# Performance work log

Hardware: AMD Instinct MI355X
Metric: run time of the kernel (lower is better)

Reference implementation:

```python
import jax, jax.numpy as jnp
import numpy as np

POS_MARGIN = 0.01
NEG_MARGIN = 0.2
REG_WEIGHT = 0.1
N, D = 8192, 256
NUM_CLASSES = 512


def setup_inputs() -> dict:
    key = jax.random.key(0)
    k1, k2 = jax.random.split(key)
    embeds = jax.random.normal(k1, (N, D), dtype=jnp.float32)
    labels = jax.random.randint(k2, (N,), 0, NUM_CLASSES, dtype=jnp.int64)
    return {"embeds": embeds, "labels": labels}


def reference(embeds, labels):
    n, d = embeds.shape
    # L2-normalize embeddings (normalize_embeds=True)
    e = embeds / jnp.linalg.norm(embeds, axis=1, keepdims=True)

    # var(e_i - e_j, ddof=1) over feature dim, computed without the [N,N,D] tensor:
    # var = (D/(D-1)) * ( mean(e_i^2) + mean(e_j^2) - 2*mean(e_i*e_j) - (m_i - m_j)^2 )
    m = e.mean(axis=1)                      # [N]
    s = (e * e).mean(axis=1)                # [N]
    g = (e @ e.T) / d                       # [N,N] = mean(e_i * e_j) over D
    corr = d / (d - 1.0)
    var_diff = corr * (s[:, None] + s[None, :] - 2.0 * g - (m[:, None] - m[None, :]) ** 2)
    row_var = corr * (s - m * m)            # torch.var(e, dim=1), unbiased
    distmat = var_diff / row_var[:, None]

    same = labels[:, None] == labels[None, :]
    eye = jnp.eye(n, dtype=bool)
    pos_mask = same & (~eye)                # all same-label pairs (anchor != positive)
    neg_mask = ~same                        # all diff-label pairs

    pos_l = jax.nn.relu(distmat - POS_MARGIN) * pos_mask
    neg_l = jax.nn.relu(NEG_MARGIN - distmat) * neg_mask

    # avg_nonzero_only=True: sum / (# strictly-positive entries + 1e-12)
    pos_loss = pos_l.sum() / ((pos_l > 0).sum().astype(jnp.float32) + 1e-12)
    neg_loss = neg_l.sum() / ((neg_l > 0).sum().astype(jnp.float32) + 1e-12)

    loss = pos_loss + neg_loss
    loss = loss + jnp.abs(e.sum(axis=1)).mean() * REG_WEIGHT
    return loss
```

## Files before the change

kernel.cpp:

```cpp
#include <hip/hip_runtime.h>

#define NROWS 8192
#define DDIM 256
#define BT 128
#define BK 32
#define GT (NROWS / BT)
#define NBT (GT * (GT + 1) / 2)

using bf16x8 = __attribute__((ext_vector_type(8))) __bf16;
using f32x4  = __attribute__((ext_vector_type(4))) float;

__device__ __forceinline__ void glds16(const unsigned short* g, unsigned short* l) {
    __builtin_amdgcn_global_load_lds(
        (const __attribute__((address_space(1))) unsigned int*)g,
        (__attribute__((address_space(3))) unsigned int*)l,
        16, 0, 0);
}

__device__ __forceinline__ unsigned short f2bf(float f) {
    unsigned int b = __float_as_uint(f);
    unsigned int r = b + 0x7fffu + ((b >> 16) & 1u);
    return (unsigned short)(r >> 16);
}

__global__ __launch_bounds__(256) void rowstats_kernel(
    const float* __restrict__ x, unsigned short* __restrict__ ebf,
    float* __restrict__ aP, float* __restrict__ bs,
    float* __restrict__ rabs)
{
    int wave = threadIdx.x >> 6;
    int lane = threadIdx.x & 63;
    int row  = blockIdx.x * 4 + wave;

    const float4 v = reinterpret_cast<const float4*>(x + (size_t)row * DDIM)[lane];
    float ss = v.x * v.x + v.y * v.y + v.z * v.z + v.w * v.w;
    float sm = v.x + v.y + v.z + v.w;
    #pragma unroll
    for (int off = 32; off >= 1; off >>= 1) {
        ss += __shfl_xor(ss, off);
        sm += __shfl_xor(sm, off);
    }
    float invn = 1.0f / sqrtf(ss);
    float m = sm * invn * (1.0f / DDIM);

    ushort4 o;
    o.x = f2bf(v.x * invn - m);
    o.y = f2bf(v.y * invn - m);
    o.z = f2bf(v.z * invn - m);
    o.w = f2bf(v.w * invn - m);
    reinterpret_cast<ushort4*>(ebf + (size_t)row * DDIM)[lane] = o;

    if (lane == 0) {
        float s  = ss * invn * invn * (1.0f / DDIM);
        float b  = s - m * m;
        float a  = 1.0f / b;
        aP[row]   = a * (1.0f / 128.0f);
        bs[row]   = -128.0f * b;
        rabs[row] = fabsf(sm * invn);
    }
}

__global__ __launch_bounds__(256) void snr_gemm_kernel(
    const unsigned short* __restrict__ ebf,
    const float* __restrict__ aP, const float* __restrict__ bs,
    const int* __restrict__ labels,
    float* __restrict__ partials)
{
    __shared__ __align__(16) unsigned short As[BT * BK];
    __shared__ __align__(16) unsigned short Bs[BT * BK];
    __shared__ float sAPi[BT], sBsi[BT];
    __shared__ float sAPj[BT], sBsj[BT];
    __shared__ int   sLi[BT], sLj[BT];
    __shared__ float redbuf[4][4];

    int tid  = threadIdx.x;
    int lane = tid & 63;
    int wave = tid >> 6;
    int wr = (wave >> 1) * 64;
    int wc = (wave & 1) * 64;

    int t = blockIdx.x;
    int bi = (int)((2.0f * GT + 1.0f
                    - sqrtf((2.0f * GT + 1.0f) * (2.0f * GT + 1.0f) - 8.0f * (float)t)) * 0.5f);
    while ((bi + 1) * GT - ((bi + 1) * bi) / 2 <= t) ++bi;
    while (bi * GT - (bi * (bi - 1)) / 2 > t) --bi;
    int bj = bi + (t - (bi * GT - (bi * (bi - 1)) / 2));
    int rowBase = bi * BT, colBase = bj * BT;
    bool diag = (bi == bj);

    if (tid < BT) {
        int gi = rowBase + tid;
        sAPi[tid] = aP[gi]; sBsi[tid] = bs[gi];
        sLi[tid] = labels[gi];
    } else {
        int tt = tid - BT;
        int gj = colBase + tt;
        sAPj[tt] = aP[gj]; sBsj[tt] = bs[gj];
        sLj[tt] = labels[gj];
    }

    const unsigned short* gA[2];
    const unsigned short* gB[2];
    unsigned short* lpA[2];
    unsigned short* lpB[2];
    #pragma unroll
    for (int p = 0; p < 2; ++p) {
        int q   = p * 256 + tid;
        int row = q >> 2;
        int kc  = (q & 3) ^ (row & 3) ^ ((row >> 2) & 3);
        gA[p] = ebf + (size_t)(rowBase + row) * DDIM + kc * 8;
        gB[p] = ebf + (size_t)(colBase + row) * DDIM + kc * 8;
        lpA[p] = As + q * 8;
        lpB[p] = Bs + q * 8;
    }

    int mrow = lane & 15;
    int kch  = lane >> 4;
    int offA[4], offB[4];
    #pragma unroll
    for (int t4 = 0; t4 < 4; ++t4) {
        int rA = wr + t4 * 16 + mrow;
        int rB = wc + t4 * 16 + mrow;
        offA[t4] = (rA * 4 + (kch ^ (rA & 3) ^ ((rA >> 2) & 3))) * 8;
        offB[t4] = (rB * 4 + (kch ^ (rB & 3) ^ ((rB >> 2) & 3))) * 8;
    }

    f32x4 acc[4][4];
    #pragma unroll
    for (int a = 0; a < 4; ++a)
        #pragma unroll
        for (int b = 0; b < 4; ++b)
            acc[a][b] = (f32x4){0.f, 0.f, 0.f, 0.f};

    for (int it = 0; it < 8; ++it) {
        #pragma unroll
        for (int p = 0; p < 2; ++p) {
            glds16(gA[p], lpA[p]);
            glds16(gB[p], lpB[p]);
            gA[p] += BK;
            gB[p] += BK;
        }
        asm volatile("s_waitcnt vmcnt(0)" ::: "memory");
        __syncthreads();

        bf16x8 aF[4], bF[4];
        #pragma unroll
        for (int t4 = 0; t4 < 4; ++t4) {
            aF[t4] = *reinterpret_cast<const bf16x8*>(As + offA[t4]);
            bF[t4] = *reinterpret_cast<const bf16x8*>(Bs + offB[t4]);
        }
        #pragma unroll
        for (int ti = 0; ti < 4; ++ti)
            #pragma unroll
            for (int tj = 0; tj < 4; ++tj)
                acc[ti][tj] = __builtin_amdgcn_mfma_f32_16x16x32_bf16(aF[ti], bF[tj], acc[ti][tj], 0, 0, 0);
        __syncthreads();
    }

    int subr = (lane >> 4) * 4;
    int cj   = lane & 15;

    float aPC[4], bsC[4];
    int LCj[4];
    #pragma unroll
    for (int tj = 0; tj < 4; ++tj) {
        int lj = wc + tj * 16 + cj;
        aPC[tj] = sAPj[lj]; bsC[tj] = sBsj[lj];
        LCj[tj] = sLj[lj];
    }

    float Sn = 0.f, Sp = 0.f;
    unsigned Cn = 0u, Cp = 0u;

    if (!diag) {
        #pragma unroll
        for (int ti = 0; ti < 4; ++ti) {
            #pragma unroll
            for (int r = 0; r < 4; ++r) {
                int li = wr + ti * 16 + subr + r;
                float aR = sAPi[li], bR = sBsi[li];
                int LR = sLi[li];
                #pragma unroll
                for (int tj = 0; tj < 4; ++tj) {
                    float raw = acc[ti][tj][r];
                    float v1 = fmaf(aR, raw + bsC[tj], -0.8f);
                    float v2 = fmaf(aPC[tj], raw + bR, -0.8f);
                    bool same = (LR == LCj[tj]);
                    unsigned long long ms = __ballot(same);
                    float nz = fmaxf(v1, 0.f) + fmaxf(v2, 0.f);
                    Sn += same ? 0.f : nz;
                    float pz = fmaxf(0.19f - v1, 0.f) + fmaxf(0.19f - v2, 0.f);
                    Sp += same ? pz : 0.f;
                    Cn += (unsigned)__popcll(__ballot(v1 > 0.f) & ~ms)
                        + (unsigned)__popcll(__ballot(v2 > 0.f) & ~ms);
                    Cp += (unsigned)__popcll(__ballot(v1 < 0.19f) & ms)
                        + (unsigned)__popcll(__ballot(v2 < 0.19f) & ms);
                }
            }
        }
    } else {
        #pragma unroll
        for (int ti = 0; ti < 4; ++ti) {
            #pragma unroll
            for (int r = 0; r < 4; ++r) {
                int li = wr + ti * 16 + subr + r;
                float aR = sAPi[li];
                int LR = sLi[li];
                #pragma unroll
                for (int tj = 0; tj < 4; ++tj) {
                    int lj = wc + tj * 16 + cj;
                    float raw = acc[ti][tj][r];
                    float v1 = fmaf(aR, raw + bsC[tj], -0.8f);
                    bool same = (LR == LCj[tj]);
                    bool pok  = same && (li != lj);
                    unsigned long long ms = __ballot(same);
                    unsigned long long mp = __ballot(pok);
                    Sn += same ? 0.f : fmaxf(v1, 0.f);
                    float pz = fmaxf(0.19f - v1, 0.f);
                    Sp += pok ? pz : 0.f;
                    Cn += (unsigned)__popcll(__ballot(v1 > 0.f) & ~ms);
                    Cp += (unsigned)__popcll(__ballot(v1 < 0.19f) & mp);
                }
            }
        }
    }

    #pragma unroll
    for (int off = 32; off >= 1; off >>= 1) {
        Sn += __shfl_down(Sn, off);
        Sp += __shfl_down(Sp, off);
    }
    if (lane == 0) {
        redbuf[wave][0] = Sn; redbuf[wave][1] = (float)Cn;
        redbuf[wave][2] = Sp; redbuf[wave][3] = (float)Cp;
    }
    __syncthreads();
    if (tid < 4) {
        partials[blockIdx.x * 4 + tid] =
            redbuf[0][tid] + redbuf[1][tid] + redbuf[2][tid] + redbuf[3][tid];
    }
}

__global__ __launch_bounds__(256) void finalize_kernel(
    const float* __restrict__ partials, const float* __restrict__ rabs,
    float* __restrict__ out)
{
    int tid = threadIdx.x;
    float s0 = 0, s1 = 0, s2 = 0, s3 = 0, rr = 0;
    for (int i = tid; i < NBT; i += 256) {
        float4 p = reinterpret_cast<const float4*>(partials)[i];
        s0 += p.x; s1 += p.y; s2 += p.z; s3 += p.w;
    }
    for (int i = tid; i < NROWS; i += 256) rr += rabs[i];

    #pragma unroll
    for (int off = 32; off >= 1; off >>= 1) {
        s0 += __shfl_down(s0, off);
        s1 += __shfl_down(s1, off);
        s2 += __shfl_down(s2, off);
        s3 += __shfl_down(s3, off);
        rr += __shfl_down(rr, off);
    }
    __shared__ float red[4][5];
    int wave = tid >> 6, lane = tid & 63;
    if (lane == 0) {
        red[wave][0] = s0; red[wave][1] = s1; red[wave][2] = s2;
        red[wave][3] = s3; red[wave][4] = rr;
    }
    __syncthreads();
    if (tid == 0) {
        float a0 = 0, a1 = 0, a2 = 0, a3 = 0, a4 = 0;
        #pragma unroll
        for (int w = 0; w < 4; ++w) {
            a0 += red[w][0]; a1 += red[w][1]; a2 += red[w][2];
            a3 += red[w][3]; a4 += red[w][4];
        }
        float neg = (a1 > 0.5f) ? a0 / (a1 + 1e-12f) : 0.0f;
        float pos = (a3 > 0.5f) ? a2 / (a3 + 1e-12f) : 0.0f;
        out[0] = pos + neg + a4 * (0.1f / (float)NROWS);
    }
}

extern "C" void kernel_launch(void* const* d_in, const int* in_sizes, int n_in,
                              void* d_out, int out_size, void* d_ws, size_t ws_size,
                              hipStream_t stream) {
    const float* embeds = (const float*)d_in[0];
    const int*   labels = (const int*)d_in[1];
    float* out = (float*)d_out;

    char* ws = (char*)d_ws;
    unsigned short* ebf = (unsigned short*)ws;
    float* aP   = (float*)(ws + (size_t)NROWS * DDIM * 2);
    float* bs   = aP + NROWS;
    float* rabs = bs + NROWS;
    float* partials = rabs + NROWS;

    rowstats_kernel<<<NROWS / 4, 256, 0, stream>>>(embeds, ebf, aP, bs, rabs);

    snr_gemm_kernel<<<NBT, 256, 0, stream>>>(ebf, aP, bs, labels, partials);

    finalize_kernel<<<1, 256, 0, stream>>>(partials, rabs, out);
}
```

Measured before the change: 124.6 us.

## Double K-tile depth to 64 and skip epilogue work for inactive wave fragments

Raises the K tile from 32 to 64, halving the number of load/sync iterations, and changes the LDS swizzle to an 8-chunk XOR pattern with two MFMA half-steps per tile. The epilogue now computes ballots for the positive-distance and same-label masks first and skips the loss accumulation when the whole wave has no contributing lanes. This trades a larger LDS footprint, possible occupancy loss and an extra branch for fewer barriers and less per-element epilogue work in the common all-zero case.

```diff
diff --git a/kernel.cpp b/kernel.cpp
--- a/kernel.cpp
+++ b/kernel.cpp
@@ -3,7 +3,7 @@
 #define NROWS 8192
 #define DDIM 256
 #define BT 128
-#define BK 32
+#define BK 64
 #define GT (NROWS / BT)
 #define NBT (GT * (GT + 1) / 2)
 
@@ -99,15 +99,15 @@
         sLj[tt] = labels[gj];
     }
 
-    const unsigned short* gA[2];
-    const unsigned short* gB[2];
-    unsigned short* lpA[2];
-    unsigned short* lpB[2];
-    #pragma unroll
-    for (int p = 0; p < 2; ++p) {
+    const unsigned short* gA[4];
+    const unsigned short* gB[4];
+    unsigned short* lpA[4];
+    unsigned short* lpB[4];
+    #pragma unroll
+    for (int p = 0; p < 4; ++p) {
         int q   = p * 256 + tid;
-        int row = q >> 2;
-        int kc  = (q & 3) ^ (row & 3) ^ ((row >> 2) & 3);
+        int row = q >> 3;
+        int kc  = (q & 7) ^ (row & 7);
         gA[p] = ebf + (size_t)(rowBase + row) * DDIM + kc * 8;
         gB[p] = ebf + (size_t)(colBase + row) * DDIM + kc * 8;
         lpA[p] = As + q * 8;
@@ -116,13 +116,16 @@
 
     int mrow = lane & 15;
     int kch  = lane >> 4;
-    int offA[4], offB[4];
+    int offA[4][2], offB[4][2];
     #pragma unroll
     for (int t4 = 0; t4 < 4; ++t4) {
         int rA = wr + t4 * 16 + mrow;
         int rB = wc + t4 * 16 + mrow;
-        offA[t4] = (rA * 4 + (kch ^ (rA & 3) ^ ((rA >> 2) & 3))) * 8;
-        offB[t4] = (rB * 4 + (kch ^ (rB & 3) ^ ((rB >> 2) & 3))) * 8;
+        #pragma unroll
+        for (int h = 0; h < 2; ++h) {
+            offA[t4][h] = (rA * 8 + ((h * 4 + kch) ^ (rA & 7))) * 8;
+            offB[t4][h] = (rB * 8 + ((h * 4 + kch) ^ (rB & 7))) * 8;
+        }
     }
 
     f32x4 acc[4][4];
@@ -132,9 +135,9 @@
         for (int b = 0; b < 4; ++b)
             acc[a][b] = (f32x4){0.f, 0.f, 0.f, 0.f};
 
-    for (int it = 0; it < 8; ++it) {
-        #pragma unroll
-        for (int p = 0; p < 2; ++p) {
+    for (int it = 0; it < 4; ++it) {
+        #pragma unroll
+        for (int p = 0; p < 4; ++p) {
             glds16(gA[p], lpA[p]);
             glds16(gB[p], lpB[p]);
             gA[p] += BK;
@@ -143,17 +146,20 @@
         asm volatile("s_waitcnt vmcnt(0)" ::: "memory");
         __syncthreads();
 
-        bf16x8 aF[4], bF[4];
-        #pragma unroll
-        for (int t4 = 0; t4 < 4; ++t4) {
-            aF[t4] = *reinterpret_cast<const bf16x8*>(As + offA[t4]);
-            bF[t4] = *reinterpret_cast<const bf16x8*>(Bs + offB[t4]);
-        }
-        #pragma unroll
-        for (int ti = 0; ti < 4; ++ti)
+        #pragma unroll
+        for (int h = 0; h < 2; ++h) {
+            bf16x8 aF[4], bF[4];
             #pragma unroll
-            for (int tj = 0; tj < 4; ++tj)
-                acc[ti][tj] = __builtin_amdgcn_mfma_f32_16x16x32_bf16(aF[ti], bF[tj], acc[ti][tj], 0, 0, 0);
+            for (int t4 = 0; t4 < 4; ++t4) {
+                aF[t4] = *reinterpret_cast<const bf16x8*>(As + offA[t4][h]);
+                bF[t4] = *reinterpret_cast<const bf16x8*>(Bs + offB[t4][h]);
+            }
+            #pragma unroll
+            for (int ti = 0; ti < 4; ++ti)
+                #pragma unroll
+                for (int tj = 0; tj < 4; ++tj)
+                    acc[ti][tj] = __builtin_amdgcn_mfma_f32_16x16x32_bf16(aF[ti], bF[tj], acc[ti][tj], 0, 0, 0);
+        }
         __syncthreads();
     }
 
@@ -186,15 +192,19 @@
                     float v1 = fmaf(aR, raw + bsC[tj], -0.8f);
                     float v2 = fmaf(aPC[tj], raw + bR, -0.8f);
                     bool same = (LR == LCj[tj]);
+                    unsigned long long b1 = __ballot(v1 > 0.f);
+                    unsigned long long b2 = __ballot(v2 > 0.f);
                     unsigned long long ms = __ballot(same);
-                    float nz = fmaxf(v1, 0.f) + fmaxf(v2, 0.f);
-                    Sn += same ? 0.f : nz;
-                    float pz = fmaxf(0.19f - v1, 0.f) + fmaxf(0.19f - v2, 0.f);
-                    Sp += same ? pz : 0.f;
-                    Cn += (unsigned)__popcll(__ballot(v1 > 0.f) & ~ms)
-                        + (unsigned)__popcll(__ballot(v2 > 0.f) & ~ms);
-                    Cp += (unsigned)__popcll(__ballot(v1 < 0.19f) & ms)
-                        + (unsigned)__popcll(__ballot(v2 < 0.19f) & ms);
+                    if (b1 | b2 | ms) {
+                        float nz = fmaxf(v1, 0.f) + fmaxf(v2, 0.f);
+                        Sn += same ? 0.f : nz;
+                        float pz = fmaxf(0.19f - v1, 0.f) + fmaxf(0.19f - v2, 0.f);
+                        Sp += same ? pz : 0.f;
+                        Cn += (unsigned)__popcll(b1 & ~ms)
+                            + (unsigned)__popcll(b2 & ~ms);
+                        Cp += (unsigned)__popcll(__ballot(v1 < 0.19f) & ms)
+                            + (unsigned)__popcll(__ballot(v2 < 0.19f) & ms);
+                    }
                 }
             }
         }
@@ -213,13 +223,16 @@
                     float v1 = fmaf(aR, raw + bsC[tj], -0.8f);
                     bool same = (LR == LCj[tj]);
                     bool pok  = same && (li != lj);
+                    unsigned long long b1 = __ballot(v1 > 0.f);
                     unsigned long long ms = __ballot(same);
-                    unsigned long long mp = __ballot(pok);
-                    Sn += same ? 0.f : fmaxf(v1, 0.f);
-                    float pz = fmaxf(0.19f - v1, 0.f);
-                    Sp += pok ? pz : 0.f;
-                    Cn += (unsigned)__popcll(__ballot(v1 > 0.f) & ~ms);
-                    Cp += (unsigned)__popcll(__ballot(v1 < 0.19f) & mp);
+                    if (b1 | ms) {
+                        unsigned long long mp = __ballot(pok);
+                        Sn += same ? 0.f : fmaxf(v1, 0.f);
+                        float pz = fmaxf(0.19f - v1, 0.f);
+                        Sp += pok ? pz : 0.f;
+                        Cn += (unsigned)__popcll(b1 & ~ms);
+                        Cp += (unsigned)__popcll(__ballot(v1 < 0.19f) & mp);
+                    }
                 }
             }
         }
```

Result: faster. 102.6 us, median of 2 (-17.7%).
